# Optimization experiments

Measured on AMD Instinct MI355X. Metric: run time of the kernel, lower is better.

The kernel has to match this reference:

```python
import jax, jax.numpy as jnp
import numpy as np

# Attention(d_model=1024, d_head=64, h=16, fastmax=True) -> fastmax_custom path with
# mask=True, normalize=True, temperature=1, a0=1, a1=1, lim=1, p=1, zero RPE.
B, N, D_MODEL, H, D_HEAD = 1, 2048, 1024, 16, 64
A0, A1, LIM = 1.0, 1.0, 1.0


def setup_inputs() -> dict:
    key = jax.random.key(0)
    ks = jax.random.split(key, 6)
    s = 1.0 / np.sqrt(D_MODEL).astype(np.float32)
    return {
        "X": jax.random.normal(ks[0], (B, N, D_MODEL), jnp.float32),
        "Wq": jax.random.normal(ks[1], (H * D_HEAD, D_MODEL), jnp.float32) * s,
        "Wk": jax.random.normal(ks[2], (H * D_HEAD, D_MODEL), jnp.float32) * s,
        "Wv": jax.random.normal(ks[3], (H * D_HEAD, D_MODEL), jnp.float32) * s,
        "Wo": jax.random.normal(ks[4], (D_MODEL, H * D_HEAD), jnp.float32) * s,
        "bo": jnp.zeros((D_MODEL,), jnp.float32),
    }


def _fastmax_causal_p1(q, k, v):
    # q,k,v: [b,h,n,d]. fastmax normalize: scale q,k so the max per-token L2 norm
    # (over the sequence, per batch-head) equals LIM; temperature forced to 1.
    qn = jnp.max(jnp.linalg.norm(q, axis=-1), axis=-1)[..., None, None]  # [b,h,1,1]
    kn = jnp.max(jnp.linalg.norm(k, axis=-1), axis=-1)[..., None, None]
    q = LIM * q / qn
    k = LIM * k / kn
    n = q.shape[2]
    # first-order (p=1) polynomial kernel attention, causal via prefix sums:
    #   score(i,j) = a0 + a1 * <q_i, k_j>,  j <= i
    kv = jnp.cumsum(k[..., :, None] * v[..., None, :], axis=2)  # [b,h,n,d,d]
    num = A0 * jnp.cumsum(v, axis=2) + A1 * jnp.einsum('bhnd,bhnde->bhne', q, kv)
    ksum = jnp.cumsum(k, axis=2)  # [b,h,n,d]
    den = A0 * jnp.arange(1, n + 1, dtype=q.dtype) + A1 * jnp.einsum('bhnd,bhnd->bhn', q, ksum)
    return num / den[..., None]


def reference(X, Wq, Wk, Wv, Wo, bo):
    b, n, _ = X.shape

    def heads(W):
        # [b,n,d_model] @ [d_model,h*d] -> [b,h,n,d]
        return (X @ W.T).reshape(b, n, H, D_HEAD).transpose(0, 2, 1, 3)

    q, k, v = heads(Wq), heads(Wk), heads(Wv)
    vh = _fastmax_causal_p1(q, k, v)                       # [b,h,n,d]
    vh = vh.transpose(0, 2, 1, 3).reshape(b, n, H * D_HEAD)
    return vh @ Wo.T + bo                                  # eval mode: dropout is identity
```

## Files before the change

### kernel.cpp

```cpp
#include <hip/hip_runtime.h>

#define N_SEQ 2048
#define NH 16
#define DH 64
#define CHUNK 64
#define NCHUNK 32

typedef float f32x4 __attribute__((ext_vector_type(4)));
typedef __bf16 bf16x8 __attribute__((ext_vector_type(8)));
typedef unsigned short u16x4 __attribute__((ext_vector_type(4)));
typedef unsigned short u16x8 __attribute__((ext_vector_type(8)));

static __device__ inline unsigned short f2b(float x) {
    unsigned int u = __builtin_bit_cast(unsigned int, x);
    unsigned int r = (u + 0x7fffu + ((u >> 16) & 1u)) >> 16;
    return (unsigned short)r;
}
static __device__ inline float b2f(unsigned short b) {
    return __builtin_bit_cast(float, (unsigned int)b << 16);
}
static __device__ inline int sw(int row, int col) {
    return row * 64 + (col ^ ((row & 7) << 3));
}

__global__ __launch_bounds__(256) void cast_all(
    const float* __restrict__ X, const float* __restrict__ Wq, const float* __restrict__ Wk,
    const float* __restrict__ Wv, const float* __restrict__ Wo,
    unsigned short* __restrict__ Xb, unsigned short* __restrict__ Wb,
    unsigned short* __restrict__ Wob, float* __restrict__ nrm) {
    if (blockIdx.x == 0 && threadIdx.x < 32) nrm[threadIdx.x] = 0.f;
    int i = blockIdx.x * 256 + threadIdx.x;
    const float* src; unsigned short* dst; int off;
    if (i < 524288)       { src = X;  dst = Xb;               off = i; }
    else if (i < 786432)  { src = Wq; dst = Wb;               off = i - 524288; }
    else if (i < 1048576) { src = Wk; dst = Wb + (1u << 20);  off = i - 786432; }
    else if (i < 1310720) { src = Wv; dst = Wb + (2u << 20);  off = i - 1048576; }
    else                  { src = Wo; dst = Wob;              off = i - 1310720; }
    float4 v = reinterpret_cast<const float4*>(src)[off];
    u16x4 o;
    o[0] = f2b(v.x); o[1] = f2b(v.y); o[2] = f2b(v.z); o[3] = f2b(v.w);
    reinterpret_cast<u16x4*>(dst)[off] = o;
}

static __device__ inline void gload_lds16(const unsigned short* g, unsigned short* l) {
    __builtin_amdgcn_global_load_lds(
        (const __attribute__((address_space(1))) unsigned int*)g,
        (__attribute__((address_space(3))) unsigned int*)l, 16, 0, 0);
}

template<int MODE, int BM>
__global__ __launch_bounds__(256, 2) void gemm_bf16(
    const unsigned short* __restrict__ A,
    const unsigned short* __restrict__ B,
    float* __restrict__ outf,
    unsigned short* __restrict__ outb,
    const float* __restrict__ bias,
    float* __restrict__ nrm,
    int M, int N, int K)
{
    __shared__ __align__(16) unsigned short As[2][BM][64];
    __shared__ __align__(16) unsigned short Bs[2][128][64];

    const int L = blockIdx.y * gridDim.x + blockIdx.x;
    const int cpx = (gridDim.x * gridDim.y) >> 3;
    const int tile = (L & 7) * cpx + (L >> 3);
    const int bn = tile / gridDim.y;
    const int bm = tile % gridDim.y;

    const int t = threadIdx.x;
    const int wave = t >> 6, lane = t & 63;
    const int wm = wave >> 1, wn = wave & 1;
    const int r16 = lane & 15, ks = lane >> 4;
    constexpr int MFRAG = BM / 32;

    f32x4 acc[MFRAG][4] = {};

    const unsigned short* gA = A + (size_t)bm * BM * K;
    const unsigned short* gB = B + (size_t)bn * 128 * K;
    const int lrow = lane >> 3;
    const int scol = (((lane & 7) ^ (lrow & 7)) << 3);
    const int rsw = (r16 & 7) << 3;
    const int NIT = K >> 6;

    auto stage = [&](int it, int pp) {
        const int k0 = it << 6;
        #pragma unroll
        for (int g2 = 0; g2 < BM / 32; ++g2) {
            int r0 = wave * (BM / 4) + g2 * 8;
            gload_lds16(&gA[(size_t)(r0 + lrow) * K + k0 + scol], &As[pp][r0][0]);
        }
        #pragma unroll
        for (int g2 = 0; g2 < 4; ++g2) {
            int r0 = wave * 32 + g2 * 8;
            gload_lds16(&gB[(size_t)(r0 + lrow) * K + k0 + scol], &Bs[pp][r0][0]);
        }
    };

    stage(0, 0);
    __syncthreads();
    int pp = 0;
    for (int it = 0; it < NIT; ++it) {
        if (it + 1 < NIT) stage(it + 1, pp ^ 1);
        #pragma unroll
        for (int ksub = 0; ksub < 2; ++ksub) {
            const int sl = (((ksub << 2) + ks) << 3) ^ rsw;
            bf16x8 af[MFRAG], bfr[4];
            #pragma unroll
            for (int m = 0; m < MFRAG; ++m)
                af[m] = *reinterpret_cast<const bf16x8*>(&As[pp][wm * (BM / 2) + m * 16 + r16][sl]);
            #pragma unroll
            for (int n = 0; n < 4; ++n)
                bfr[n] = *reinterpret_cast<const bf16x8*>(&Bs[pp][wn * 64 + n * 16 + r16][sl]);
            #pragma unroll
            for (int m = 0; m < MFRAG; ++m)
                #pragma unroll
                for (int n = 0; n < 4; ++n)
                    acc[m][n] = __builtin_amdgcn_mfma_f32_16x16x32_bf16(af[m], bfr[n], acc[m][n], 0, 0, 0);
        }
        pp ^= 1;
        if (it + 1 < NIT) __syncthreads();
    }

    #pragma unroll
    for (int m = 0; m < MFRAG; ++m) {
        int row0 = bm * BM + wm * (BM / 2) + m * 16 + ks * 4;
        #pragma unroll
        for (int n = 0; n < 4; ++n) {
            int col = bn * 128 + wn * 64 + n * 16 + r16;
            if (MODE == 0) {
                int wch = col >> 10, h = (col >> 6) & 15, d = col & 63;
                unsigned short* dst = outb + (size_t)wch * (NH * (size_t)N_SEQ * DH)
                                          + (size_t)h * N_SEQ * DH + d;
                #pragma unroll
                for (int j = 0; j < 4; ++j)
                    dst[(size_t)(row0 + j) * DH] = f2b(acc[m][n][j]);
            } else {
                float bv = bias[col];
                #pragma unroll
                for (int j = 0; j < 4; ++j)
                    outf[(size_t)(row0 + j) * N + col] = acc[m][n][j] + bv;
            }
        }
    }

    if (MODE == 0) {
        const int colbase = bn * 128 + wn * 64;
        const int wch = colbase >> 10;
        if (wch < 2) {
            const int h = (colbase >> 6) & 15;
            float mx = 0.f;
            #pragma unroll
            for (int m = 0; m < MFRAG; ++m)
                #pragma unroll
                for (int j = 0; j < 4; ++j) {
                    float rs = 0.f;
                    #pragma unroll
                    for (int n = 0; n < 4; ++n) rs = fmaf(acc[m][n][j], acc[m][n][j], rs);
                    rs += __shfl_xor(rs, 1);
                    rs += __shfl_xor(rs, 2);
                    rs += __shfl_xor(rs, 4);
                    rs += __shfl_xor(rs, 8);
                    mx = fmaxf(mx, rs);
                }
            mx = fmaxf(mx, __shfl_xor(mx, 16));
            mx = fmaxf(mx, __shfl_xor(mx, 32));
            if (lane == 0)
                atomicMax(reinterpret_cast<unsigned int*>(&nrm[wch * 16 + h]),
                          __builtin_bit_cast(unsigned int, mx));
        }
    }
}

__global__ __launch_bounds__(256) void chunk_sums(const unsigned short* __restrict__ Kb,
                                                  const unsigned short* __restrict__ Vb,
                                                  unsigned short* __restrict__ Ssum,
                                                  float* __restrict__ zsum,
                                                  float* __restrict__ vssum) {
    const int h = blockIdx.x >> 5, c = blockIdx.x & 31;
    __shared__ __align__(16) unsigned short Kt[4096];
    __shared__ __align__(16) unsigned short Vt[4096];
    const size_t off = ((size_t)h * N_SEQ + c * CHUNK) * DH;
    const int t = threadIdx.x, lane = t & 63;

    {
        const int d = t & 63, j0 = (t >> 6) * 16;
        unsigned short rk[16], rv[16];
        #pragma unroll
        for (int i = 0; i < 16; ++i) {
            rk[i] = Kb[off + (size_t)(j0 + i) * DH + d];
            rv[i] = Vb[off + (size_t)(j0 + i) * DH + d];
        }
        u16x8 a, b;
        #pragma unroll
        for (int i = 0; i < 8; ++i) { a[i] = rk[i]; b[i] = rk[8 + i]; }
        *reinterpret_cast<u16x8*>(&Kt[sw(d, j0)]) = a;
        *reinterpret_cast<u16x8*>(&Kt[sw(d, j0 + 8)]) = b;
        #pragma unroll
        for (int i = 0; i < 8; ++i) { a[i] = rv[i]; b[i] = rv[8 + i]; }
        *reinterpret_cast<u16x8*>(&Vt[sw(d, j0)]) = a;
        *reinterpret_cast<u16x8*>(&Vt[sw(d, j0 + 8)]) = b;
    }
    __syncthreads();

    const int w = t >> 6, cl = lane & 15, g = lane >> 4;
    bf16x8 ak0 = *reinterpret_cast<const bf16x8*>(&Kt[sw(w * 16 + cl, g * 8)]);
    bf16x8 ak1 = *reinterpret_cast<const bf16x8*>(&Kt[sw(w * 16 + cl, 32 + g * 8)]);
    f32x4 acc[4] = {};
    #pragma unroll
    for (int et = 0; et < 4; ++et) {
        bf16x8 b0 = *reinterpret_cast<const bf16x8*>(&Vt[sw(et * 16 + cl, g * 8)]);
        bf16x8 b1 = *reinterpret_cast<const bf16x8*>(&Vt[sw(et * 16 + cl, 32 + g * 8)]);
        acc[et] = __builtin_amdgcn_mfma_f32_16x16x32_bf16(ak0, b0, acc[et], 0, 0, 0);
        acc[et] = __builtin_amdgcn_mfma_f32_16x16x32_bf16(ak1, b1, acc[et], 0, 0, 0);
    }
    unsigned short* So = Ssum + (size_t)blockIdx.x * (DH * DH);
    #pragma unroll
    for (int et = 0; et < 4; ++et)
        #pragma unroll
        for (int j = 0; j < 4; ++j)
            So[(size_t)(w * 16 + g * 4 + j) * DH + et * 16 + cl] = f2b(acc[et][j]);

    if (t < 64) {
        float z = 0.f;
        #pragma unroll
        for (int i = 0; i < 8; ++i) {
            u16x8 v = *reinterpret_cast<const u16x8*>(&Kt[sw(t, i * 8)]);
            #pragma unroll
            for (int k = 0; k < 8; ++k) z += b2f(v[k]);
        }
        zsum[(size_t)blockIdx.x * DH + t] = z;
    } else if (t < 128) {
        int e = t - 64;
        float z = 0.f;
        #pragma unroll
        for (int i = 0; i < 8; ++i) {
            u16x8 v = *reinterpret_cast<const u16x8*>(&Vt[sw(e, i * 8)]);
            #pragma unroll
            for (int k = 0; k < 8; ++k) z += b2f(v[k]);
        }
        vssum[(size_t)blockIdx.x * DH + e] = z;
    }
}

__global__ __launch_bounds__(256) void chunk_scan(unsigned short* __restrict__ Ssum,
                                                  float* __restrict__ zsum,
                                                  float* __restrict__ vssum) {
    const int b = blockIdx.x;
    if (b < 256) {
        const int h = b >> 4;
        const int e = (b & 15) * 256 + threadIdx.x;
        size_t base = (size_t)h * NCHUNK * (DH * DH) + e;
        float run = 0.f;
        for (int c = 0; c < NCHUNK; ++c) {
            size_t idx = base + (size_t)c * (DH * DH);
            float tmp = b2f(Ssum[idx]); Ssum[idx] = f2b(run); run += tmp;
        }
    } else {
        const int g = (b - 256) * 256 + threadIdx.x;
        const int which = g >> 10, h = (g >> 6) & 15, e = g & 63;
        float* arr = which ? vssum : zsum;
        size_t base = (size_t)h * NCHUNK * DH + e;
        float run = 0.f;
        for (int c = 0; c < NCHUNK; ++c) {
            size_t idx = base + (size_t)c * DH;
            float tmp = arr[idx]; arr[idx] = run; run += tmp;
        }
    }
}

__global__ __launch_bounds__(256) void intra_attn(
    const unsigned short* __restrict__ Qb, const unsigned short* __restrict__ Kb,
    const unsigned short* __restrict__ Vb,
    const unsigned short* __restrict__ Ssum, const float* __restrict__ zsum,
    const float* __restrict__ vssum, const float* __restrict__ nrm,
    unsigned short* __restrict__ vhb) {
    const int h = blockIdx.x >> 5, c = blockIdx.x & 31;
    __shared__ __align__(16) unsigned short Ql[4096];
    __shared__ __align__(16) unsigned short Kl[4096];
    __shared__ __align__(16) unsigned short Vt[4096];
    __shared__ __align__(16) unsigned short Sp[4096];
    __shared__ __align__(16) unsigned short Pl[4096];
    __shared__ float zp[DH], vsp[DH];

    const int t = threadIdx.x, lane = t & 63, w = t >> 6;
    const float alpha = 1.f / sqrtf(nrm[h] * nrm[16 + h]);
    const size_t off = ((size_t)h * N_SEQ + c * CHUNK) * DH;

    #pragma unroll
    for (int p = 0; p < 2; ++p) {
        int lin = t + p * 256;
        int row = lin >> 3, col = (lin & 7) * 8;
        u16x8 q = *reinterpret_cast<const u16x8*>(Qb + off + (size_t)row * DH + col);
        u16x8 k = *reinterpret_cast<const u16x8*>(Kb + off + (size_t)row * DH + col);
        *reinterpret_cast<u16x8*>(&Ql[sw(row, col)]) = q;
        *reinterpret_cast<u16x8*>(&Kl[sw(row, col)]) = k;
    }
    {
        const int e = t & 63, j0 = (t >> 6) * 16;
        unsigned short rv[16];
        #pragma unroll
        for (int i = 0; i < 16; ++i) rv[i] = Vb[off + (size_t)(j0 + i) * DH + e];
        u16x8 a, b;
        #pragma unroll
        for (int i = 0; i < 8; ++i) { a[i] = rv[i]; b[i] = rv[8 + i]; }
        *reinterpret_cast<u16x8*>(&Vt[sw(e, j0)]) = a;
        *reinterpret_cast<u16x8*>(&Vt[sw(e, j0 + 8)]) = b;
    }
    {
        const unsigned short* Sg = Ssum + (size_t)blockIdx.x * (DH * DH);
        const int e = t & 63, d0 = (t >> 6) * 16;
        u16x8 a, b;
        #pragma unroll
        for (int i = 0; i < 8; ++i) a[i] = f2b(alpha * b2f(Sg[(size_t)(d0 + i) * DH + e]));
        #pragma unroll
        for (int i = 0; i < 8; ++i) b[i] = f2b(alpha * b2f(Sg[(size_t)(d0 + 8 + i) * DH + e]));
        *reinterpret_cast<u16x8*>(&Sp[sw(e, d0)]) = a;
        *reinterpret_cast<u16x8*>(&Sp[sw(e, d0 + 8)]) = b;
    }
    if (t < 64) zp[t] = alpha * zsum[(size_t)blockIdx.x * DH + t];
    else if (t < 128) vsp[t - 64] = vssum[(size_t)blockIdx.x * DH + (t - 64)];
    __syncthreads();

    const int cl = lane & 15, g = lane >> 4;
    const int qrow = (w << 4) + cl;

    bf16x8 aq0 = *reinterpret_cast<const bf16x8*>(&Ql[sw(qrow, g * 8)]);
    bf16x8 aq1 = *reinterpret_cast<const bf16x8*>(&Ql[sw(qrow, 32 + g * 8)]);

    f32x4 acc[4] = {};
    #pragma unroll
    for (int et = 0; et < 4; ++et) {
        bf16x8 b0 = *reinterpret_cast<const bf16x8*>(&Sp[sw(et * 16 + cl, g * 8)]);
        bf16x8 b1 = *reinterpret_cast<const bf16x8*>(&Sp[sw(et * 16 + cl, 32 + g * 8)]);
        acc[et] = __builtin_amdgcn_mfma_f32_16x16x32_bf16(aq0, b0, acc[et], 0, 0, 0);
        acc[et] = __builtin_amdgcn_mfma_f32_16x16x32_bf16(aq1, b1, acc[et], 0, 0, 0);
    }
    f32x4 sacc[4] = {};
    #pragma unroll
    for (int kt = 0; kt < 4; ++kt) {
        bf16x8 b0 = *reinterpret_cast<const bf16x8*>(&Kl[sw(kt * 16 + cl, g * 8)]);
        bf16x8 b1 = *reinterpret_cast<const bf16x8*>(&Kl[sw(kt * 16 + cl, 32 + g * 8)]);
        sacc[kt] = __builtin_amdgcn_mfma_f32_16x16x32_bf16(aq0, b0, sacc[kt], 0, 0, 0);
        sacc[kt] = __builtin_amdgcn_mfma_f32_16x16x32_bf16(aq1, b1, sacc[kt], 0, 0, 0);
    }
    unsigned short* Pw = &Pl[w * 1024];
    float part[4] = {0.f, 0.f, 0.f, 0.f};
    #pragma unroll
    for (int kt = 0; kt < 4; ++kt) {
        int key = kt * 16 + cl;
        #pragma unroll
        for (int j = 0; j < 4; ++j) {
            int rr = g * 4 + j;
            int q = (w << 4) + rr;
            float s = (key <= q) ? fmaf(alpha, sacc[kt][j], 1.f) : 0.f;
            part[j] += s;
            Pw[rr * 64 + (key ^ ((rr & 7) << 3))] = f2b(s);
        }
    }
    #pragma unroll
    for (int j = 0; j < 4; ++j) {
        int q = (w << 4) + g * 4 + j;
        float qz = 0.f;
        #pragma unroll
        for (int m = 0; m < 4; ++m) {
            int d = cl + m * 16;
            qz = fmaf(b2f(Ql[sw(q, d)]), zp[d], qz);
        }
        part[j] += qz;
    }
    #pragma unroll
    for (int o = 1; o < 16; o <<= 1)
        #pragma unroll
        for (int j = 0; j < 4; ++j) part[j] += __shfl_xor(part[j], o);
    float invden[4];
    #pragma unroll
    for (int j = 0; j < 4; ++j) invden[j] = 1.f / ((float)(c * CHUNK) + part[j]);

    #pragma unroll
    for (int ks = 0; ks < 2; ++ks) {
        bf16x8 ap = *reinterpret_cast<const bf16x8*>(&Pw[cl * 64 + ((ks * 32 + g * 8) ^ ((cl & 7) << 3))]);
        #pragma unroll
        for (int et = 0; et < 4; ++et) {
            bf16x8 bv = *reinterpret_cast<const bf16x8*>(&Vt[sw(et * 16 + cl, ks * 32 + g * 8)]);
            acc[et] = __builtin_amdgcn_mfma_f32_16x16x32_bf16(ap, bv, acc[et], 0, 0, 0);
        }
    }
    #pragma unroll
    for (int et = 0; et < 4; ++et)
        #pragma unroll
        for (int j = 0; j < 4; ++j) {
            int q = (w << 4) + g * 4 + j;
            int e = et * 16 + cl;
            float o = (vsp[e] + acc[et][j]) * invden[j];
            vhb[(size_t)(c * CHUNK + q) * (NH * DH) + h * DH + e] = f2b(o);
        }
}

extern "C" void kernel_launch(void* const* d_in, const int* in_sizes, int n_in,
                              void* d_out, int out_size, void* d_ws, size_t ws_size,
                              hipStream_t stream) {
    const float* X  = (const float*)d_in[0];
    const float* Wq = (const float*)d_in[1];
    const float* Wk = (const float*)d_in[2];
    const float* Wv = (const float*)d_in[3];
    const float* Wo = (const float*)d_in[4];
    const float* bo = (const float*)d_in[5];
    float* out = (float*)d_out;

    char* w = (char*)d_ws;
    unsigned short* Xb   = (unsigned short*)(w);
    unsigned short* Wb   = (unsigned short*)(w + (4u  << 20));
    unsigned short* Wob  = (unsigned short*)(w + (10u << 20));
    unsigned short* Qb   = (unsigned short*)(w + (12u << 20));
    unsigned short* vhb  = (unsigned short*)(w + (24u << 20));
    float*          nrm  = (float*)(w + (28u << 20));
    unsigned short* Ssum = (unsigned short*)(w + (29u << 20));
    float*          zsum = (float*)(w + (34u << 20));
    float*          vssum= (float*)(w + (34u << 20) + (1u << 17));
    unsigned short* Kb = Qb + 2097152;
    unsigned short* Vb = Qb + 2u * 2097152;

    cast_all<<<6144, 256, 0, stream>>>(X, Wq, Wk, Wv, Wo, Xb, Wb, Wob, nrm);
    gemm_bf16<0, 128><<<dim3(24, 16), 256, 0, stream>>>(Xb, Wb, nullptr, Qb, nullptr, nrm, 2048, 3072, 1024);
    chunk_sums<<<512, 256, 0, stream>>>(Kb, Vb, Ssum, zsum, vssum);
    chunk_scan<<<264, 256, 0, stream>>>(Ssum, zsum, vssum);
    intra_attn<<<512, 256, 0, stream>>>(Qb, Kb, Vb, Ssum, zsum, vssum, nrm, vhb);
    gemm_bf16<1, 64><<<dim3(8, 32), 256, 0, stream>>>(vhb, Wob, out, nullptr, bo, nullptr, 2048, 1024, 1024);
}
```

Baseline: 69.08 us.

## Fuse chunk prefix scan into intra_attn and refine GEMM pipeline sync

Removes the separate chunk_scan kernel. Each intra_attn block now sums the preceding chunks' KV state, z sums and v sums directly from global memory. This saves a kernel launch and a serial scan pass, but adds redundant O(c) reads per block, which weigh most on late chunks. The GEMM main loop also swaps __syncthreads for explicit vmcnt/lgkmcnt waits with raw barriers, so the prefetch of the next stage can stay in flight while the current tile is computed.

```diff
diff --git a/kernel.cpp b/kernel.cpp
--- a/kernel.cpp
+++ b/kernel.cpp
@@ -72,6 +72,7 @@
     const int wm = wave >> 1, wn = wave & 1;
     const int r16 = lane & 15, ks = lane >> 4;
     constexpr int MFRAG = BM / 32;
+    constexpr int STG = BM / 32 + 4;
 
     f32x4 acc[MFRAG][4] = {};
 
@@ -97,10 +98,17 @@
     };
 
     stage(0, 0);
-    __syncthreads();
     int pp = 0;
     for (int it = 0; it < NIT; ++it) {
-        if (it + 1 < NIT) stage(it + 1, pp ^ 1);
+        if (it + 1 < NIT) {
+            stage(it + 1, pp ^ 1);
+            asm volatile("s_waitcnt vmcnt(%0)" :: "i"(STG) : "memory");
+        } else {
+            asm volatile("s_waitcnt vmcnt(0)" ::: "memory");
+        }
+        __builtin_amdgcn_s_barrier();
+        __builtin_amdgcn_sched_barrier(0);
+
         #pragma unroll
         for (int ksub = 0; ksub < 2; ++ksub) {
             const int sl = (((ksub << 2) + ks) << 3) ^ rsw;
@@ -117,8 +125,9 @@
                 for (int n = 0; n < 4; ++n)
                     acc[m][n] = __builtin_amdgcn_mfma_f32_16x16x32_bf16(af[m], bfr[n], acc[m][n], 0, 0, 0);
         }
+        asm volatile("s_waitcnt lgkmcnt(0)" ::: "memory");
+        __builtin_amdgcn_s_barrier();
         pp ^= 1;
-        if (it + 1 < NIT) __syncthreads();
     }
 
     #pragma unroll
@@ -242,32 +251,6 @@
     }
 }
 
-__global__ __launch_bounds__(256) void chunk_scan(unsigned short* __restrict__ Ssum,
-                                                  float* __restrict__ zsum,
-                                                  float* __restrict__ vssum) {
-    const int b = blockIdx.x;
-    if (b < 256) {
-        const int h = b >> 4;
-        const int e = (b & 15) * 256 + threadIdx.x;
-        size_t base = (size_t)h * NCHUNK * (DH * DH) + e;
-        float run = 0.f;
-        for (int c = 0; c < NCHUNK; ++c) {
-            size_t idx = base + (size_t)c * (DH * DH);
-            float tmp = b2f(Ssum[idx]); Ssum[idx] = f2b(run); run += tmp;
-        }
-    } else {
-        const int g = (b - 256) * 256 + threadIdx.x;
-        const int which = g >> 10, h = (g >> 6) & 15, e = g & 63;
-        float* arr = which ? vssum : zsum;
-        size_t base = (size_t)h * NCHUNK * DH + e;
-        float run = 0.f;
-        for (int c = 0; c < NCHUNK; ++c) {
-            size_t idx = base + (size_t)c * DH;
-            float tmp = arr[idx]; arr[idx] = run; run += tmp;
-        }
-    }
-}
-
 __global__ __launch_bounds__(256) void intra_attn(
     const unsigned short* __restrict__ Qb, const unsigned short* __restrict__ Kb,
     const unsigned short* __restrict__ Vb,
@@ -307,18 +290,33 @@
         *reinterpret_cast<u16x8*>(&Vt[sw(e, j0 + 8)]) = b;
     }
     {
-        const unsigned short* Sg = Ssum + (size_t)blockIdx.x * (DH * DH);
         const int e = t & 63, d0 = (t >> 6) * 16;
+        float accS[16];
+        #pragma unroll
+        for (int i = 0; i < 16; ++i) accS[i] = 0.f;
+        const unsigned short* Sg = Ssum + (size_t)(h * NCHUNK) * (DH * DH);
+        for (int cc = 0; cc < c; ++cc) {
+            const unsigned short* Sc = Sg + (size_t)cc * (DH * DH);
+            #pragma unroll
+            for (int i = 0; i < 16; ++i) accS[i] += b2f(Sc[(size_t)(d0 + i) * DH + e]);
+        }
         u16x8 a, b;
         #pragma unroll
-        for (int i = 0; i < 8; ++i) a[i] = f2b(alpha * b2f(Sg[(size_t)(d0 + i) * DH + e]));
-        #pragma unroll
-        for (int i = 0; i < 8; ++i) b[i] = f2b(alpha * b2f(Sg[(size_t)(d0 + 8 + i) * DH + e]));
+        for (int i = 0; i < 8; ++i) a[i] = f2b(alpha * accS[i]);
+        #pragma unroll
+        for (int i = 0; i < 8; ++i) b[i] = f2b(alpha * accS[8 + i]);
         *reinterpret_cast<u16x8*>(&Sp[sw(e, d0)]) = a;
         *reinterpret_cast<u16x8*>(&Sp[sw(e, d0 + 8)]) = b;
     }
-    if (t < 64) zp[t] = alpha * zsum[(size_t)blockIdx.x * DH + t];
-    else if (t < 128) vsp[t - 64] = vssum[(size_t)blockIdx.x * DH + (t - 64)];
+    if (t < 64) {
+        float z = 0.f;
+        for (int cc = 0; cc < c; ++cc) z += zsum[(size_t)(h * NCHUNK + cc) * DH + t];
+        zp[t] = alpha * z;
+    } else if (t < 128) {
+        float z = 0.f;
+        for (int cc = 0; cc < c; ++cc) z += vssum[(size_t)(h * NCHUNK + cc) * DH + (t - 64)];
+        vsp[t - 64] = z;
+    }
     __syncthreads();
 
     const int cl = lane & 15, g = lane >> 4;
@@ -423,7 +421,6 @@
     cast_all<<<6144, 256, 0, stream>>>(X, Wq, Wk, Wv, Wo, Xb, Wb, Wob, nrm);
     gemm_bf16<0, 128><<<dim3(24, 16), 256, 0, stream>>>(Xb, Wb, nullptr, Qb, nullptr, nrm, 2048, 3072, 1024);
     chunk_sums<<<512, 256, 0, stream>>>(Kb, Vb, Ssum, zsum, vssum);
-    chunk_scan<<<264, 256, 0, stream>>>(Ssum, zsum, vssum);
     intra_attn<<<512, 256, 0, stream>>>(Qb, Kb, Vb, Ssum, zsum, vssum, nrm, vhb);
     gemm_bf16<1, 64><<<dim3(8, 32), 256, 0, stream>>>(vhb, Wob, out, nullptr, bo, nullptr, 2048, 1024, 1024);
 }
```

Measured after the change: 80.02 us. 1.16x slower.
